# Performance work log

Hardware: AMD Instinct MI355X
Metric: run time of the kernel (lower is better)

## Reference

```python
import jax, jax.numpy as jnp
import numpy as np

# dims derived from init_kwargs
N_NODES = 100000            # type_mask.shape[0]
N0, N1 = 60000, 40000       # nodes per type
F0, F1 = 128, 64            # feats_dim_list
HID = 64                    # hidden_dim (= in_dim of layer1)
HEADS = 8
OUT = 16
ATTN_VEC = 128
E = 250000                  # metapath instances per metapath
L = 3                       # nodes per metapath instance (2 edge types)
NG = 8192                   # nodes in each minibatch DGL graph
B = 8192                    # number of target nodes
ETYPES = [[0, 1], [2, 3]]   # etypes_list; num_edge_type=4, RotatE0 -> 2 base relations


def setup_inputs() -> dict:
    ks = jax.random.split(jax.random.key(0), 20)
    g = lambda k, s, sc=1.0: sc * jax.random.normal(k, s, dtype=jnp.float32)
    return {
        "feat0": g(ks[0], (N0, F0)),
        "feat1": g(ks[1], (N1, F1)),
        "W0": g(ks[2], (HID, F0), 0.12),
        "b0": jnp.zeros((HID,), jnp.float32),
        "W1": g(ks[3], (HID, F1), 0.15),
        "b1": jnp.zeros((HID,), jnp.float32),
        "r_vec": g(ks[4], (2, HID // 2, 2), 0.2),
        "attn0": g(ks[5], (HEADS, HID), 0.2),
        "attn1": g(ks[6], (HEADS, HID), 0.2),
        "fc1_w": g(ks[7], (ATTN_VEC, HEADS * HID), 0.06),
        "fc1_b": jnp.zeros((ATTN_VEC,), jnp.float32),
        "fc2_w": g(ks[8], (1, ATTN_VEC), 0.1),
        "fc_w": g(ks[9], (OUT, HEADS * HID), 0.06),
        "fc_b": jnp.zeros((OUT,), jnp.float32),
        "idx0": jnp.arange(N0, dtype=jnp.int32),                 # type-0 node ids (contiguous block)
        "idx1": jnp.arange(N1, dtype=jnp.int32) + N0,            # type-1 node ids (offset block)
        "mp0_indices": jax.random.randint(ks[10], (E, L), 0, N_NODES, dtype=jnp.int32),
        "mp0_dst": jax.random.randint(ks[11], (E,), 0, NG, dtype=jnp.int32),
        "mp0_target": jax.random.randint(ks[12], (B,), 0, NG, dtype=jnp.int32),
        "mp1_indices": jax.random.randint(ks[13], (E, L), 0, N_NODES, dtype=jnp.int32),
        "mp1_dst": jax.random.randint(ks[14], (E,), 0, NG, dtype=jnp.int32),
        "mp1_target": jax.random.randint(ks[15], (B,), 0, NG, dtype=jnp.int32),
    }


def _cmul(a, b):
    # complex multiply on trailing dim of size 2
    re = a[..., 0] * b[..., 0] - a[..., 1] * b[..., 1]
    im = a[..., 0] * b[..., 1] + a[..., 1] * b[..., 0]
    return jnp.stack([re, im], axis=-1)


def reference(feat0, feat1, W0, b0, W1, b1, r_vec, attn0, attn1,
              fc1_w, fc1_b, fc2_w, fc_w, fc_b,
              idx0, idx1,
              mp0_indices, mp0_dst, mp0_target,
              mp1_indices, mp1_dst, mp1_target):
    # per-node-type linear scattered into a dense [N, HID] table (dropout=0 / eval)
    tf = jnp.zeros((N_NODES, HID), jnp.float32)
    tf = tf.at[idx0].set(feat0 @ W0.T + b0)
    tf = tf.at[idx1].set(feat1 @ W1.T + b1)

    # RotatE0: unit-modulus normalize, then double relations with conjugates
    rv = r_vec / jnp.linalg.norm(r_vec, axis=-1, keepdims=True)          # [2, HID//2, 2]
    conj = rv * jnp.array([1.0, -1.0], rv.dtype)
    rv_full = jnp.stack([rv, conj], axis=1).reshape(-1, HID // 2, 2)     # [4, HID//2, 2]

    def metapath(indices, dst, target, attn, etypes):
        edata = tf[indices].reshape(E, L, HID // 2, 2)   # gather metapath instances
        # suffix products of rotations: final[i] = prod_{j>=i} r[etypes[j]], final[L-1]=1
        final = [jnp.stack([jnp.ones(HID // 2, jnp.float32),
                            jnp.zeros(HID // 2, jnp.float32)], -1)]
        for i in range(L - 2, -1, -1):
            final.insert(0, _cmul(final[0], rv_full[etypes[i]]))
        finals = jnp.stack(final, axis=0)                # [L, HID//2, 2]
        edata = _cmul(edata, finals)                     # rotate every path position
        h = edata.reshape(E, L, HID).mean(axis=1)        # [E, HID] instance encoding
        # node-level attention (heads share h: torch tiles hidden across heads)
        a = jax.nn.leaky_relu(h @ attn.T, 0.01)          # [E, HEADS]
        m = jax.ops.segment_max(a, dst, num_segments=NG)
        ex = jnp.exp(a - m[dst])
        s = jax.ops.segment_sum(ex, dst, num_segments=NG)
        an = ex / s[dst]                                 # edge softmax per destination
        eft = jnp.einsum('eh,ed->ehd', an, h)            # [E, HEADS, HID]
        ft = jax.ops.segment_sum(eft, dst, num_segments=NG)
        ret = ft[target].reshape(B, HEADS * HID)
        return jax.nn.elu(ret)

    out0 = metapath(mp0_indices, mp0_dst, mp0_target, attn0, ETYPES[0])
    out1 = metapath(mp1_indices, mp1_dst, mp1_target, attn1, ETYPES[1])

    # metapath-level attention
    outs = jnp.stack([out0, out1], axis=0)               # [P, B, HEADS*HID]
    s1 = jnp.tanh(outs @ fc1_w.T + fc1_b)                # [P, B, ATTN_VEC]
    beta = jax.nn.softmax((s1.mean(axis=1) @ fc2_w.T)[:, 0], axis=0)  # [P]
    hagg = jnp.einsum('p,pbf->bf', beta, outs)           # [B, HEADS*HID]
    logits = hagg @ fc_w.T + fc_b                        # [B, OUT]
    return logits, hagg
```

## Files before the change

kernel.cpp:

```cpp
#include <hip/hip_runtime.h>
#include <hip/hip_fp16.h>
#include <math.h>

#define NNODES 100000
#define NT0 60000
#define NT1 40000
#define FD0 128
#define FD1 64
#define HID 64
#define HEADS 8
#define OUTD 16
#define AVEC 128
#define NE 250000
#define NG 8192
#define NB 8192

typedef _Float16 half8v __attribute__((ext_vector_type(8)));
typedef float f32x4 __attribute__((ext_vector_type(4)));

#define OFF_TF16    0ull
#define OFF_FINALS  3200000ull
#define OFF_A       3200512ull
#define OFF_ACC     3203584ull
#define OFF_BETA    3203840ull
#define OFF_FC1H    3204096ull
#define OFF_P       3236864ull
#define OFF_SORTED  5636864ull
#define OFF_COUNTS  7636864ull
#define OFF_CNTT    7653248ull
#define OFF_CURS    7669632ull
#define OFF_OFFS    7686016ull
#define OFF_FT16    7702656ull

__global__ __launch_bounds__(256) void k_prep(const float* __restrict__ r_vec,
                       const float* __restrict__ attn0, const float* __restrict__ attn1,
                       float* __restrict__ finals, float* __restrict__ A,
                       float* __restrict__ acc, float* __restrict__ beta){
  __shared__ float2 fl[192];
  int t = threadIdx.x;
  if (t < 32){
    int j = t;
    const float2* rv = (const float2*)r_vec;
    float2 r0 = rv[j];
    float2 r1 = rv[32 + j];
    float n0 = rsqrtf(r0.x*r0.x + r0.y*r0.y);
    float n1 = rsqrtf(r1.x*r1.x + r1.y*r1.y);
    r0.x *= n0; r0.y *= n0; r1.x *= n1; r1.y *= n1;
    float2 rf1 = make_float2(r0.x, -r0.y);
    float2 rf3 = make_float2(r1.x, -r1.y);
    float2 F00 = make_float2(rf1.x*r0.x - rf1.y*r0.y, rf1.x*r0.y + rf1.y*r0.x);
    float2 F10 = make_float2(rf3.x*r1.x - rf3.y*r1.y, rf3.x*r1.y + rf3.y*r1.x);
    float2 one = make_float2(1.f, 0.f);
    float2* F = (float2*)finals;
    F[0*32+j] = F00; F[1*32+j] = rf1; F[2*32+j] = one;
    F[3*32+j] = F10; F[4*32+j] = rf3; F[5*32+j] = one;
    fl[0*32+j] = F00; fl[1*32+j] = rf1; fl[2*32+j] = one;
    fl[3*32+j] = F10; fl[4*32+j] = rf3; fl[5*32+j] = one;
  }
  __syncthreads();
  for (int idx = t; idx < 1536; idx += 256){
    int pair = idx & 31, k = (idx >> 5) & 7, pi = idx >> 8;
    const float* at = (pi >= 3) ? attn1 : attn0;
    float2 f = fl[pi*32 + pair];
    float a0 = at[k*64 + 2*pair], a1 = at[k*64 + 2*pair + 1];
    A[(pi*8+k)*64 + 2*pair]     = (f.x*a0 + f.y*a1) * (1.f/3.f);
    A[(pi*8+k)*64 + 2*pair + 1] = (f.x*a1 - f.y*a0) * (1.f/3.f);
  }
  acc[t] = 0.f;
  if (t < 2) beta[t] = 0.f;
}

__global__ void k_cvtw(const float* __restrict__ fc1_w, __half* __restrict__ fc1h){
  int t = blockIdx.x*blockDim.x + threadIdx.x;
  fc1h[t] = __float2half(fc1_w[t]);
}

__global__ __launch_bounds__(256) void k_transform2(const float* __restrict__ feat0,
                  const float* __restrict__ W0v, const float* __restrict__ b0v,
                  const int* __restrict__ idx0,
                  const float* __restrict__ feat1, const float* __restrict__ W1v,
                  const float* __restrict__ b1v, const int* __restrict__ idx1,
                  __half* __restrict__ tf16){
  __shared__ float An[64][34];
  __shared__ float Bn[64][34];
  const int nb0 = (NT0 + 63)/64;
  int bid = blockIdx.x;
  const float *feat, *W, *bias; const int* idx; int n_nodes, F, m0;
  if (bid < nb0){ feat=feat0; W=W0v; bias=b0v; idx=idx0; n_nodes=NT0; F=FD0; m0=bid*64; }
  else { feat=feat1; W=W1v; bias=b1v; idx=idx1; n_nodes=NT1; F=FD1; m0=(bid-nb0)*64; }
  int t = threadIdx.x;
  int tx = t & 15;
  int ty = t >> 4;
  int Fq = F >> 2;

  float acc[4][4];
  #pragma unroll
  for (int i = 0; i < 4; ++i)
    #pragma unroll
    for (int j = 0; j < 4; ++j) acc[i][j] = 0.f;

  const float4* feat4 = (const float4*)feat;
  const float4* W4 = (const float4*)W;

  for (int k0 = 0; k0 < F; k0 += 32){
    #pragma unroll
    for (int qq = 0; qq < 2; ++qq){
      int q = t + qq*256;
      int m = q >> 3, kq = q & 7;
      int gm = m0 + m; if (gm > n_nodes - 1) gm = n_nodes - 1;
      float4 v = feat4[(size_t)gm*Fq + (k0 >> 2) + kq];
      *(float2*)&An[m][kq*4]     = make_float2(v.x, v.y);
      *(float2*)&An[m][kq*4 + 2] = make_float2(v.z, v.w);
    }
    #pragma unroll
    for (int qq = 0; qq < 2; ++qq){
      int q = t + qq*256;
      int d = q >> 3, kq = q & 7;
      float4 v = W4[(size_t)d*Fq + (k0 >> 2) + kq];
      *(float2*)&Bn[d][kq*4]     = make_float2(v.x, v.y);
      *(float2*)&Bn[d][kq*4 + 2] = make_float2(v.z, v.w);
    }
    __syncthreads();
    #pragma unroll 8
    for (int kk2 = 0; kk2 < 16; ++kk2){
      float2 a2[4], b2[4];
      #pragma unroll
      for (int i = 0; i < 4; ++i) a2[i] = *(const float2*)&An[tx + 16*i][kk2*2];
      #pragma unroll
      for (int j = 0; j < 4; ++j) b2[j] = *(const float2*)&Bn[ty*4 + j][kk2*2];
      #pragma unroll
      for (int i = 0; i < 4; ++i)
        #pragma unroll
        for (int j = 0; j < 4; ++j)
          acc[i][j] += a2[i].x*b2[j].x + a2[i].y*b2[j].y;
    }
    __syncthreads();
  }

  float4 bv = *(const float4*)&bias[ty*4];
  #pragma unroll
  for (int i = 0; i < 4; ++i){
    int gm = m0 + tx + 16*i;
    if (gm < n_nodes){
      union { __half2 h2[2]; uint2 u; } pk;
      pk.h2[0] = __floats2half2_rn(acc[i][0] + bv.x, acc[i][1] + bv.y);
      pk.h2[1] = __floats2half2_rn(acc[i][2] + bv.z, acc[i][3] + bv.w);
      *(uint2*)&tf16[(size_t)idx[gm]*HID + ty*4] = pk.u;
    }
  }
}

__global__ __launch_bounds__(256) void k_pmat(const __half* __restrict__ tf16,
                                              const float* __restrict__ A,
                                              __half* __restrict__ P){
  __shared__ float tfl[64][65];
  __shared__ float Al[48][65];
  int t = threadIdx.x;
  int n0 = blockIdx.x * 64;
  for (int q = t; q < 3072; q += 256) Al[q >> 6][q & 63] = A[q];
  const __half2* tfh = (const __half2*)(tf16 + (size_t)n0*64);
  for (int q = t; q < 2048; q += 256){
    int n = q >> 5, dq = q & 31;
    float2 v = make_float2(0.f, 0.f);
    if (n0 + n < NNODES) v = __half22float2(tfh[n*32 + dq]);
    tfl[n][dq*2] = v.x; tfl[n][dq*2+1] = v.y;
  }
  __syncthreads();
  int nl = t >> 2, q = t & 3;
  float s[12];
  #pragma unroll
  for (int c = 0; c < 12; ++c) s[c] = 0.f;
  #pragma unroll 4
  for (int d = 0; d < 64; ++d){
    float tv = tfl[nl][d];
    #pragma unroll
    for (int c = 0; c < 12; ++c) s[c] += tv * Al[q*12 + c][d];
  }
  int gn = n0 + nl;
  if (gn < NNODES){
    #pragma unroll
    for (int c = 0; c < 12; ++c){
      int cg = q*12 + c;
      int p = cg >= 24;
      int w = cg - p*24;
      P[(size_t)p*2400000 + (size_t)gn*24 + w] = __float2half(s[c]);
    }
  }
}

__global__ void k_zeroi(int* __restrict__ p, int n){
  int t = blockIdx.x*blockDim.x + threadIdx.x;
  if (t < n) p[t] = 0;
}

__global__ void k_hist3(const int* __restrict__ d0, const int* __restrict__ d1,
                        const int* __restrict__ t0, const int* __restrict__ t1,
                        int* __restrict__ counts, int* __restrict__ cntt){
  int e = blockIdx.x*blockDim.x + threadIdx.x;
  if (e < NE) atomicAdd(&counts[d0[e]], 1);
  else if (e < 2*NE) atomicAdd(&counts[NG + d1[e-NE]], 1);
  else if (e < 2*NE + NB) atomicAdd(&cntt[t0[e-2*NE]], 1);
  else if (e < 2*NE + 2*NB) atomicAdd(&cntt[NG + t1[e-2*NE-NB]], 1);
}

__global__ __launch_bounds__(1024) void k_scan(const int* __restrict__ counts,
                                               int* __restrict__ offs,
                                               int* __restrict__ curs){
  __shared__ int lds[1024];
  int t = threadIdx.x;
  int base = t*16;
  int v[16]; int sum = 0;
  #pragma unroll
  for (int i = 0; i < 16; ++i){ v[i] = counts[base+i]; sum += v[i]; }
  lds[t] = sum;
  __syncthreads();
  for (int off = 1; off < 1024; off <<= 1){
    int x = (t >= off) ? lds[t-off] : 0;
    __syncthreads();
    lds[t] += x;
    __syncthreads();
  }
  int excl = lds[t] - sum;
  #pragma unroll
  for (int i = 0; i < 16; ++i){ offs[base+i] = excl; excl += v[i]; curs[base+i] = 0; }
  if (t == 1023) offs[2*NG] = excl;
}

__global__ void k_scatter2(const int* __restrict__ m0, const int* __restrict__ d0,
                           const int* __restrict__ m1, const int* __restrict__ d1,
                           const int* __restrict__ offs, int* __restrict__ curs,
                           int4* __restrict__ sorted){
  int e = blockIdx.x*blockDim.x + threadIdx.x;
  if (e >= 2*NE) return;
  const int* mp; int d;
  if (e < NE){ mp = m0 + (size_t)e*3; d = d0[e]; }
  else { mp = m1 + (size_t)(e-NE)*3; d = NG + d1[e-NE]; }
  int pos = offs[d] + atomicAdd(&curs[d], 1);
  sorted[pos] = make_int4(mp[0], mp[1], mp[2], 0);
}

__global__ __launch_bounds__(64) void k_seg(const __half* __restrict__ tf16,
                                            const __half* __restrict__ P,
                                            const int4* __restrict__ sorted,
                                            const int* __restrict__ offs,
                                            const float* __restrict__ finals,
                                            __half* __restrict__ ft16o){
  int bid = blockIdx.x;
  int p = bid >> 13;
  int lane = threadIdx.x;
  int hw = lane >> 5, j = lane & 31;
  int start = offs[bid], end = offs[bid+1];
  __half2* ftw = (__half2*)(ft16o + (size_t)bid*512);
  if (start == end){
    #pragma unroll
    for (int kk = 0; kk < 4; ++kk) ftw[(hw*4+kk)*32 + j] = __floats2half2_rn(0.f, 0.f);
    return;
  }
  const float2* F2 = (const float2*)(finals + p*192);
  float2 f0 = F2[j], f1 = F2[32 + j];
  const __half2* tfh = (const __half2*)tf16;
  const __half* Pp = P + (size_t)p*2400000;

  __shared__ int4 ndb[64];
  __shared__ float wb[64][8];

  float s[8], ur[8], ui[8];
  #pragma unroll
  for (int k = 0; k < 8; ++k){ s[k] = 0.f; ur[k] = 0.f; ui[k] = 0.f; }

  for (int c = start; c < end; c += 64){
    int n = end - c; if (n > 64) n = 64;
    if (lane < n){
      int4 nd = sorted[c + lane];
      ndb[lane] = nd;
      float4 rA = *(const float4*)(Pp + (size_t)nd.x*24);
      float4 rB = *(const float4*)(Pp + (size_t)nd.y*24 + 8);
      float4 rC = *(const float4*)(Pp + (size_t)nd.z*24 + 16);
      const __half2* ha = (const __half2*)&rA;
      const __half2* hb = (const __half2*)&rB;
      const __half2* hc = (const __half2*)&rC;
      float w[8];
      #pragma unroll
      for (int m = 0; m < 4; ++m){
        float2 va = __half22float2(ha[m]);
        float2 vb = __half22float2(hb[m]);
        float2 vc = __half22float2(hc[m]);
        float x0 = va.x + vb.x + vc.x;
        float x1 = va.y + vb.y + vc.y;
        x0 = x0 > 0.f ? x0 : 0.01f*x0;
        x1 = x1 > 0.f ? x1 : 0.01f*x1;
        w[2*m]   = __expf(x0);
        w[2*m+1] = __expf(x1);
      }
      *(float4*)&wb[lane][0] = make_float4(w[0], w[1], w[2], w[3]);
      *(float4*)&wb[lane][4] = make_float4(w[4], w[5], w[6], w[7]);
    }
    __syncthreads();
    int cend = c + n;
    for (int i = c + hw; i < cend; i += 2){
      int e = i - c;
      int4 nd = ndb[e];
      float4 wlo = *(const float4*)&wb[e][0];
      float4 whi = *(const float4*)&wb[e][4];
      float2 v0 = __half22float2(tfh[(size_t)nd.x*32 + j]);
      float2 v1 = __half22float2(tfh[(size_t)nd.y*32 + j]);
      float2 v2 = __half22float2(tfh[(size_t)nd.z*32 + j]);
      float hre = (v0.x*f0.x - v0.y*f0.y) + (v1.x*f1.x - v1.y*f1.y) + v2.x;
      float him = (v0.x*f0.y + v0.y*f0.x) + (v1.x*f1.y + v1.y*f1.x) + v2.y;
      ur[0] += wlo.x*hre; ui[0] += wlo.x*him; s[0] += wlo.x;
      ur[1] += wlo.y*hre; ui[1] += wlo.y*him; s[1] += wlo.y;
      ur[2] += wlo.z*hre; ui[2] += wlo.z*him; s[2] += wlo.z;
      ur[3] += wlo.w*hre; ui[3] += wlo.w*him; s[3] += wlo.w;
      ur[4] += whi.x*hre; ui[4] += whi.x*him; s[4] += whi.x;
      ur[5] += whi.y*hre; ui[5] += whi.y*him; s[5] += whi.y;
      ur[6] += whi.z*hre; ui[6] += whi.z*him; s[6] += whi.z;
      ur[7] += whi.w*hre; ui[7] += whi.w*him; s[7] += whi.w;
    }
    __syncthreads();
  }
  #pragma unroll
  for (int k = 0; k < 8; ++k){
    ur[k] += __shfl_xor(ur[k], 32);
    ui[k] += __shfl_xor(ui[k], 32);
    s[k]  += __shfl_xor(s[k], 32);
  }
  #pragma unroll
  for (int kk = 0; kk < 4; ++kk){
    int k = hw*4 + kk;
    float inv = 1.f / (3.f * s[k]);
    float re = ur[k]*inv, im = ui[k]*inv;
    re = re > 0.f ? re : expm1f(re);
    im = im > 0.f ? im : expm1f(im);
    ftw[k*32 + j] = __floats2half2_rn(re, im);
  }
}

__global__ __launch_bounds__(256) void k_s1g(const __half* __restrict__ ft16o,
                                             const int* __restrict__ cntt,
                                             const __half* __restrict__ fc1h,
                                             const float* __restrict__ fc1_b,
                                             float* __restrict__ acc_p){
  int bid = blockIdx.x;
  int p  = bid >> 8;
  int rb = bid & 255;
  int t = threadIdx.x;
  int w = t >> 6, l = t & 63;
  int rowbase = rb*32 + (w & 1)*16;
  int colbase = (w >> 1)*64;
  int lr = l & 15, lk = l >> 4;

  const half8v* Ab = (const half8v*)(ft16o + ((size_t)p*NG + rowbase)*512);
  f32x4 acc[4] = {{0.f,0.f,0.f,0.f},{0.f,0.f,0.f,0.f},
                  {0.f,0.f,0.f,0.f},{0.f,0.f,0.f,0.f}};

  #pragma unroll 4
  for (int kk = 0; kk < 16; ++kk){
    half8v a = Ab[(size_t)lr*64 + kk*4 + lk];
    #pragma unroll
    for (int ct = 0; ct < 4; ++ct){
      const half8v* Bb = (const half8v*)(fc1h + (size_t)(colbase + ct*16 + lr)*512);
      half8v b = Bb[kk*4 + lk];
      acc[ct] = __builtin_amdgcn_mfma_f32_16x16x32_f16(a, b, acc[ct], 0, 0, 0);
    }
  }

  float cf[4];
  #pragma unroll
  for (int r = 0; r < 4; ++r)
    cf[r] = (float)cntt[p*NG + rowbase + lk*4 + r];
  #pragma unroll
  for (int ct = 0; ct < 4; ++ct){
    int col = colbase + ct*16 + lr;
    float bv = fc1_b[col];
    float sv = 0.f;
    #pragma unroll
    for (int r = 0; r < 4; ++r)
      sv += cf[r] * tanhf(acc[ct][r] + bv);
    sv += __shfl_xor(sv, 16);
    sv += __shfl_xor(sv, 32);
    if (l < 16) atomicAdd(&acc_p[p*128 + col], sv);
  }
}

__global__ void k_beta(const float* __restrict__ acc, const float* __restrict__ fc2_w,
                       float* __restrict__ beta){
  int t = threadIdx.x;
  float s0 = acc[t]*fc2_w[t] + acc[t+64]*fc2_w[t+64];
  float s1 = acc[128+t]*fc2_w[t] + acc[192+t]*fc2_w[t+64];
  #pragma unroll
  for (int mask = 1; mask < 64; mask <<= 1){
    s0 += __shfl_xor(s0, mask, 64);
    s1 += __shfl_xor(s1, mask, 64);
  }
  if (t == 0){
    float z0 = s0 / (float)NB, z1 = s1 / (float)NB;
    float mz = fmaxf(z0, z1);
    float e0 = expf(z0 - mz), e1 = expf(z1 - mz);
    float inv = 1.f / (e0 + e1);
    beta[0] = e0*inv; beta[1] = e1*inv;
  }
}

__global__ void k_final(const __half* __restrict__ ft0, const __half* __restrict__ ft1,
                        const int* __restrict__ tgt0, const int* __restrict__ tgt1,
                        const float* __restrict__ beta, const float* __restrict__ fc_w,
                        const float* __restrict__ fc_b, float* __restrict__ d_out){
  __shared__ float lds[512];
  int b = blockIdx.x, t = threadIdx.x;
  float b0 = beta[0], b1 = beta[1];
  int g0 = tgt0[b], g1 = tgt1[b];
  float v0 = __half2float(ft0[(size_t)g0*512 + t]);
  float v1 = __half2float(ft1[(size_t)g1*512 + t]);
  float h = b0*v0 + b1*v1;
  lds[t] = h;
  d_out[(size_t)NB*OUTD + (size_t)b*512 + t] = h;
  __syncthreads();
  int o = t >> 5, j = t & 31;
  float s = 0.f;
  const float* w = fc_w + o*512;
  for (int d = j; d < 512; d += 32) s += lds[d]*w[d];
  #pragma unroll
  for (int mask = 1; mask < 32; mask <<= 1) s += __shfl_xor(s, mask, 32);
  if (j == 0) d_out[(size_t)b*OUTD + o] = s + fc_b[o];
}

extern "C" void kernel_launch(void* const* d_in, const int* in_sizes, int n_in,
                              void* d_out, int out_size, void* d_ws, size_t ws_size,
                              hipStream_t stream){
  const float* feat0  = (const float*)d_in[0];
  const float* feat1  = (const float*)d_in[1];
  const float* W0     = (const float*)d_in[2];
  const float* b0     = (const float*)d_in[3];
  const float* W1     = (const float*)d_in[4];
  const float* b1     = (const float*)d_in[5];
  const float* r_vec  = (const float*)d_in[6];
  const float* attn0  = (const float*)d_in[7];
  const float* attn1  = (const float*)d_in[8];
  const float* fc1_w  = (const float*)d_in[9];
  const float* fc1_b  = (const float*)d_in[10];
  const float* fc2_w  = (const float*)d_in[11];
  const float* fc_w   = (const float*)d_in[12];
  const float* fc_b   = (const float*)d_in[13];
  const int*   idx0   = (const int*)d_in[14];
  const int*   idx1   = (const int*)d_in[15];
  const int*   mpi0   = (const int*)d_in[16];
  const int*   mdst0  = (const int*)d_in[17];
  const int*   mtgt0  = (const int*)d_in[18];
  const int*   mpi1   = (const int*)d_in[19];
  const int*   mdst1  = (const int*)d_in[20];
  const int*   mtgt1  = (const int*)d_in[21];

  float* ws      = (float*)d_ws;
  __half* tf16   = (__half*)(ws + OFF_TF16);
  float* finals  = ws + OFF_FINALS;
  float* Amat    = ws + OFF_A;
  float* acc     = ws + OFF_ACC;
  float* beta    = ws + OFF_BETA;
  __half* fc1h   = (__half*)(ws + OFF_FC1H);
  __half* P      = (__half*)(ws + OFF_P);
  int4*  sorted  = (int4*)(ws + OFF_SORTED);
  int*   counts  = (int*)(ws + OFF_COUNTS);
  int*   cntt    = (int*)(ws + OFF_CNTT);
  int*   curs    = (int*)(ws + OFF_CURS);
  int*   offs    = (int*)(ws + OFF_OFFS);
  __half* ft16o  = (__half*)(ws + OFF_FT16);
  __half* ft0h   = ft16o;
  __half* ft1h   = ft16o + (size_t)NG*512;

  k_prep<<<1, 256, 0, stream>>>(r_vec, attn0, attn1, finals, Amat, acc, beta);
  k_cvtw<<<256, 256, 0, stream>>>(fc1_w, fc1h);
  k_zeroi<<<128, 256, 0, stream>>>(counts, 4*NG);
  k_hist3<<<(2*NE + 2*NB + 255)/256, 256, 0, stream>>>(mdst0, mdst1, mtgt0, mtgt1,
                                                       counts, cntt);
  k_scan<<<1, 1024, 0, stream>>>(counts, offs, curs);
  k_scatter2<<<(2*NE + 255)/256, 256, 0, stream>>>(mpi0, mdst0, mpi1, mdst1,
                                                   offs, curs, sorted);

  k_transform2<<<(NT0 + 63)/64 + (NT1 + 63)/64, 256, 0, stream>>>(
      feat0, W0, b0, idx0, feat1, W1, b1, idx1, tf16);
  k_pmat<<<(NNODES + 63)/64, 256, 0, stream>>>(tf16, Amat, P);

  k_seg<<<2*NG, 64, 0, stream>>>(tf16, P, sorted, offs, finals, ft16o);

  k_s1g<<<512, 256, 0, stream>>>(ft16o, cntt, fc1h, fc1_b, acc);
  k_beta<<<1, 64, 0, stream>>>(acc, fc2_w, beta);
  k_final<<<NB, 512, 0, stream>>>(ft0h, ft1h, mtgt0, mtgt1, beta, fc_w, fc_b,
                                  (float*)d_out);
}
```

Baseline: 254.9 us.

## Fold attention projection into transform weights and compute with MFMA

```diff
diff --git a/kernel.cpp b/kernel.cpp
--- a/kernel.cpp
+++ b/kernel.cpp
@@ -20,23 +20,30 @@
 
 #define OFF_TF16    0ull
 #define OFF_FINALS  3200000ull
-#define OFF_A       3200512ull
-#define OFF_ACC     3203584ull
-#define OFF_BETA    3203840ull
-#define OFF_FC1H    3204096ull
-#define OFF_P       3236864ull
-#define OFF_SORTED  5636864ull
-#define OFF_COUNTS  7636864ull
-#define OFF_CNTT    7653248ull
-#define OFF_CURS    7669632ull
-#define OFF_OFFS    7686016ull
-#define OFF_FT16    7702656ull
-
-__global__ __launch_bounds__(256) void k_prep(const float* __restrict__ r_vec,
-                       const float* __restrict__ attn0, const float* __restrict__ attn1,
-                       float* __restrict__ finals, float* __restrict__ A,
-                       float* __restrict__ acc, float* __restrict__ beta){
+#define OFF_ACC     3200512ull
+#define OFF_BETA    3200768ull
+#define OFF_WC0     3201024ull
+#define OFF_WC1     3208192ull
+#define OFF_BC0     3211776ull
+#define OFF_BC1     3211904ull
+#define OFF_FC1H    3212032ull
+#define OFF_P       3244800ull
+#define OFF_SORTED  5644800ull
+#define OFF_COUNTS  7644800ull
+#define OFF_CNTT    7661184ull
+#define OFF_CURS    7677568ull
+#define OFF_OFFS    7693952ull
+#define OFF_FT16    7710592ull
+
+__global__ __launch_bounds__(256) void k_wprep(const float* __restrict__ r_vec,
+     const float* __restrict__ attn0, const float* __restrict__ attn1,
+     const float* __restrict__ W0v, const float* __restrict__ b0v,
+     const float* __restrict__ W1v, const float* __restrict__ b1v,
+     float* __restrict__ finals, __half* __restrict__ wc0, float* __restrict__ bc0,
+     __half* __restrict__ wc1, float* __restrict__ bc1,
+     float* __restrict__ acc, float* __restrict__ beta){
   __shared__ float2 fl[192];
+  __shared__ float Ash[48][66];
   int t = threadIdx.x;
   if (t < 32){
     int j = t;
@@ -63,8 +70,46 @@
     const float* at = (pi >= 3) ? attn1 : attn0;
     float2 f = fl[pi*32 + pair];
     float a0 = at[k*64 + 2*pair], a1 = at[k*64 + 2*pair + 1];
-    A[(pi*8+k)*64 + 2*pair]     = (f.x*a0 + f.y*a1) * (1.f/3.f);
-    A[(pi*8+k)*64 + 2*pair + 1] = (f.x*a1 - f.y*a0) * (1.f/3.f);
+    Ash[pi*8+k][2*pair]     = (f.x*a0 + f.y*a1) * (1.f/3.f);
+    Ash[pi*8+k][2*pair + 1] = (f.x*a1 - f.y*a0) * (1.f/3.f);
+  }
+  __syncthreads();
+  for (int q = t; q < 112*128; q += 256){
+    int c = q >> 7, f = q & 127;
+    float v;
+    if (c < 64) v = W0v[c*128 + f];
+    else {
+      float s = 0.f;
+      #pragma unroll 8
+      for (int d = 0; d < 64; ++d) s += Ash[c-64][d] * W0v[d*128 + f];
+      v = s;
+    }
+    wc0[q] = __float2half(v);
+  }
+  for (int q = t; q < 112*64; q += 256){
+    int c = q >> 6, f = q & 63;
+    float v;
+    if (c < 64) v = W1v[c*64 + f];
+    else {
+      float s = 0.f;
+      #pragma unroll 8
+      for (int d = 0; d < 64; ++d) s += Ash[c-64][d] * W1v[d*64 + f];
+      v = s;
+    }
+    wc1[q] = __float2half(v);
+  }
+  if (t < 112){
+    float s0, s1;
+    if (t < 64){ s0 = b0v[t]; s1 = b1v[t]; }
+    else {
+      s0 = 0.f; s1 = 0.f;
+      #pragma unroll 8
+      for (int d = 0; d < 64; ++d){
+        s0 += Ash[t-64][d] * b0v[d];
+        s1 += Ash[t-64][d] * b1v[d];
+      }
+    }
+    bc0[t] = s0; bc1[t] = s1;
   }
   acc[t] = 0.f;
   if (t < 2) beta[t] = 0.f;
@@ -75,115 +120,66 @@
   fc1h[t] = __float2half(fc1_w[t]);
 }
 
-__global__ __launch_bounds__(256) void k_transform2(const float* __restrict__ feat0,
-                  const float* __restrict__ W0v, const float* __restrict__ b0v,
-                  const int* __restrict__ idx0,
-                  const float* __restrict__ feat1, const float* __restrict__ W1v,
-                  const float* __restrict__ b1v, const int* __restrict__ idx1,
-                  __half* __restrict__ tf16){
-  __shared__ float An[64][34];
-  __shared__ float Bn[64][34];
+__global__ __launch_bounds__(256) void k_tform(const float* __restrict__ feat0,
+      const int* __restrict__ idx0, const float* __restrict__ feat1,
+      const int* __restrict__ idx1,
+      const __half* __restrict__ wc0, const float* __restrict__ bc0,
+      const __half* __restrict__ wc1, const float* __restrict__ bc1,
+      __half* __restrict__ tf16, __half* __restrict__ P){
   const int nb0 = (NT0 + 63)/64;
   int bid = blockIdx.x;
-  const float *feat, *W, *bias; const int* idx; int n_nodes, F, m0;
-  if (bid < nb0){ feat=feat0; W=W0v; bias=b0v; idx=idx0; n_nodes=NT0; F=FD0; m0=bid*64; }
-  else { feat=feat1; W=W1v; bias=b1v; idx=idx1; n_nodes=NT1; F=FD1; m0=(bid-nb0)*64; }
+  const float* feat; const int* idx; const __half* wc; const float* bc;
+  int n_nodes, F, m0;
+  if (bid < nb0){ feat=feat0; idx=idx0; wc=wc0; bc=bc0; n_nodes=NT0; F=FD0; m0=bid*64; }
+  else { feat=feat1; idx=idx1; wc=wc1; bc=bc1; n_nodes=NT1; F=FD1; m0=(bid-nb0)*64; }
+  __shared__ int idxs[64];
   int t = threadIdx.x;
-  int tx = t & 15;
-  int ty = t >> 4;
-  int Fq = F >> 2;
-
-  float acc[4][4];
-  #pragma unroll
-  for (int i = 0; i < 4; ++i)
-    #pragma unroll
-    for (int j = 0; j < 4; ++j) acc[i][j] = 0.f;
-
-  const float4* feat4 = (const float4*)feat;
-  const float4* W4 = (const float4*)W;
-
-  for (int k0 = 0; k0 < F; k0 += 32){
-    #pragma unroll
-    for (int qq = 0; qq < 2; ++qq){
-      int q = t + qq*256;
-      int m = q >> 3, kq = q & 7;
-      int gm = m0 + m; if (gm > n_nodes - 1) gm = n_nodes - 1;
-      float4 v = feat4[(size_t)gm*Fq + (k0 >> 2) + kq];
-      *(float2*)&An[m][kq*4]     = make_float2(v.x, v.y);
-      *(float2*)&An[m][kq*4 + 2] = make_float2(v.z, v.w);
-    }
-    #pragma unroll
-    for (int qq = 0; qq < 2; ++qq){
-      int q = t + qq*256;
-      int d = q >> 3, kq = q & 7;
-      float4 v = W4[(size_t)d*Fq + (k0 >> 2) + kq];
-      *(float2*)&Bn[d][kq*4]     = make_float2(v.x, v.y);
-      *(float2*)&Bn[d][kq*4 + 2] = make_float2(v.z, v.w);
-    }
-    __syncthreads();
-    #pragma unroll 8
-    for (int kk2 = 0; kk2 < 16; ++kk2){
-      float2 a2[4], b2[4];
-      #pragma unroll
-      for (int i = 0; i < 4; ++i) a2[i] = *(const float2*)&An[tx + 16*i][kk2*2];
-      #pragma unroll
-      for (int j = 0; j < 4; ++j) b2[j] = *(const float2*)&Bn[ty*4 + j][kk2*2];
-      #pragma unroll
-      for (int i = 0; i < 4; ++i)
-        #pragma unroll
-        for (int j = 0; j < 4; ++j)
-          acc[i][j] += a2[i].x*b2[j].x + a2[i].y*b2[j].y;
-    }
-    __syncthreads();
-  }
-
-  float4 bv = *(const float4*)&bias[ty*4];
-  #pragma unroll
-  for (int i = 0; i < 4; ++i){
-    int gm = m0 + tx + 16*i;
-    if (gm < n_nodes){
-      union { __half2 h2[2]; uint2 u; } pk;
-      pk.h2[0] = __floats2half2_rn(acc[i][0] + bv.x, acc[i][1] + bv.y);
-      pk.h2[1] = __floats2half2_rn(acc[i][2] + bv.z, acc[i][3] + bv.w);
-      *(uint2*)&tf16[(size_t)idx[gm]*HID + ty*4] = pk.u;
-    }
-  }
-}
-
-__global__ __launch_bounds__(256) void k_pmat(const __half* __restrict__ tf16,
-                                              const float* __restrict__ A,
-                                              __half* __restrict__ P){
-  __shared__ float tfl[64][65];
-  __shared__ float Al[48][65];
-  int t = threadIdx.x;
-  int n0 = blockIdx.x * 64;
-  for (int q = t; q < 3072; q += 256) Al[q >> 6][q & 63] = A[q];
-  const __half2* tfh = (const __half2*)(tf16 + (size_t)n0*64);
-  for (int q = t; q < 2048; q += 256){
-    int n = q >> 5, dq = q & 31;
-    float2 v = make_float2(0.f, 0.f);
-    if (n0 + n < NNODES) v = __half22float2(tfh[n*32 + dq]);
-    tfl[n][dq*2] = v.x; tfl[n][dq*2+1] = v.y;
+  if (t < 64){
+    int gm = m0 + t; if (gm > n_nodes - 1) gm = n_nodes - 1;
+    idxs[t] = idx[gm];
   }
   __syncthreads();
-  int nl = t >> 2, q = t & 3;
-  float s[12];
-  #pragma unroll
-  for (int c = 0; c < 12; ++c) s[c] = 0.f;
-  #pragma unroll 4
-  for (int d = 0; d < 64; ++d){
-    float tv = tfl[nl][d];
-    #pragma unroll
-    for (int c = 0; c < 12; ++c) s[c] += tv * Al[q*12 + c][d];
-  }
-  int gn = n0 + nl;
-  if (gn < NNODES){
-    #pragma unroll
-    for (int c = 0; c < 12; ++c){
-      int cg = q*12 + c;
-      int p = cg >= 24;
-      int w = cg - p*24;
-      P[(size_t)p*2400000 + (size_t)gn*24 + w] = __float2half(s[c]);
+  int w = t >> 6, l = t & 63;
+  int lr = l & 15, lk = l >> 4;
+  int gr = m0 + w*16 + lr; if (gr > n_nodes - 1) gr = n_nodes - 1;
+  const float* arow = feat + (size_t)gr*F;
+
+  f32x4 acc7[7];
+  #pragma unroll
+  for (int ct = 0; ct < 7; ++ct) acc7[ct] = (f32x4){0.f,0.f,0.f,0.f};
+
+  int nk = F >> 5;
+  for (int kk = 0; kk < nk; ++kk){
+    int koff = kk*32 + lk*8;
+    float4 ua = *(const float4*)(arow + koff);
+    float4 ub = *(const float4*)(arow + koff + 4);
+    half8v a = {(_Float16)ua.x,(_Float16)ua.y,(_Float16)ua.z,(_Float16)ua.w,
+                (_Float16)ub.x,(_Float16)ub.y,(_Float16)ub.z,(_Float16)ub.w};
+    #pragma unroll
+    for (int ct = 0; ct < 7; ++ct){
+      half8v b = *(const half8v*)(wc + (size_t)(ct*16 + lr)*F + koff);
+      acc7[ct] = __builtin_amdgcn_mfma_f32_16x16x32_f16(a, b, acc7[ct], 0, 0, 0);
+    }
+  }
+
+  #pragma unroll
+  for (int ct = 0; ct < 7; ++ct){
+    int col = ct*16 + lr;
+    float bv = bc[col];
+    #pragma unroll
+    for (int r = 0; r < 4; ++r){
+      int nl = w*16 + lk*4 + r;
+      int gm = m0 + nl;
+      if (gm < n_nodes){
+        __half hv = __float2half(acc7[ct][r] + bv);
+        int gn = idxs[nl];
+        if (col < 64) tf16[(size_t)gn*64 + col] = hv;
+        else {
+          int cg = col - 64;
+          int p = cg >= 24;
+          P[(size_t)p*2400000 + (size_t)gn*24 + (cg - p*24)] = hv;
+        }
+      }
     }
   }
 }
@@ -264,9 +260,9 @@
   __shared__ int4 ndb[64];
   __shared__ float wb[64][8];
 
-  float s[8], ur[8], ui[8];
-  #pragma unroll
-  for (int k = 0; k < 8; ++k){ s[k] = 0.f; ur[k] = 0.f; ui[k] = 0.f; }
+  float sA[8], ur[8], ui[8];
+  #pragma unroll
+  for (int k = 0; k < 8; ++k){ sA[k] = 0.f; ur[k] = 0.f; ui[k] = 0.f; }
 
   for (int c = start; c < end; c += 64){
     int n = end - c; if (n > 64) n = 64;
@@ -292,6 +288,8 @@
         w[2*m]   = __expf(x0);
         w[2*m+1] = __expf(x1);
       }
+      #pragma unroll
+      for (int k = 0; k < 8; ++k) sA[k] += w[k];
       *(float4*)&wb[lane][0] = make_float4(w[0], w[1], w[2], w[3]);
       *(float4*)&wb[lane][4] = make_float4(w[4], w[5], w[6], w[7]);
     }
@@ -307,14 +305,14 @@
       float2 v2 = __half22float2(tfh[(size_t)nd.z*32 + j]);
       float hre = (v0.x*f0.x - v0.y*f0.y) + (v1.x*f1.x - v1.y*f1.y) + v2.x;
       float him = (v0.x*f0.y + v0.y*f0.x) + (v1.x*f1.y + v1.y*f1.x) + v2.y;
-      ur[0] += wlo.x*hre; ui[0] += wlo.x*him; s[0] += wlo.x;
-      ur[1] += wlo.y*hre; ui[1] += wlo.y*him; s[1] += wlo.y;
-      ur[2] += wlo.z*hre; ui[2] += wlo.z*him; s[2] += wlo.z;
-      ur[3] += wlo.w*hre; ui[3] += wlo.w*him; s[3] += wlo.w;
-      ur[4] += whi.x*hre; ui[4] += whi.x*him; s[4] += whi.x;
-      ur[5] += whi.y*hre; ui[5] += whi.y*him; s[5] += whi.y;
-      ur[6] += whi.z*hre; ui[6] += whi.z*him; s[6] += whi.z;
-      ur[7] += whi.w*hre; ui[7] += whi.w*him; s[7] += whi.w;
+      ur[0] += wlo.x*hre; ui[0] += wlo.x*him;
+      ur[1] += wlo.y*hre; ui[1] += wlo.y*him;
+      ur[2] += wlo.z*hre; ui[2] += wlo.z*him;
+      ur[3] += wlo.w*hre; ui[3] += wlo.w*him;
+      ur[4] += whi.x*hre; ui[4] += whi.x*him;
+      ur[5] += whi.y*hre; ui[5] += whi.y*him;
+      ur[6] += whi.z*hre; ui[6] += whi.z*him;
+      ur[7] += whi.w*hre; ui[7] += whi.w*him;
     }
     __syncthreads();
   }
@@ -322,12 +320,15 @@
   for (int k = 0; k < 8; ++k){
     ur[k] += __shfl_xor(ur[k], 32);
     ui[k] += __shfl_xor(ui[k], 32);
-    s[k]  += __shfl_xor(s[k], 32);
+    float v = sA[k];
+    #pragma unroll
+    for (int mask = 1; mask < 64; mask <<= 1) v += __shfl_xor(v, mask);
+    sA[k] = v;
   }
   #pragma unroll
   for (int kk = 0; kk < 4; ++kk){
     int k = hw*4 + kk;
-    float inv = 1.f / (3.f * s[k]);
+    float inv = 1.f / (3.f * sA[k]);
     float re = ur[k]*inv, im = ui[k]*inv;
     re = re > 0.f ? re : expm1f(re);
     im = im > 0.f ? im : expm1f(im);
@@ -453,9 +454,12 @@
   float* ws      = (float*)d_ws;
   __half* tf16   = (__half*)(ws + OFF_TF16);
   float* finals  = ws + OFF_FINALS;
-  float* Amat    = ws + OFF_A;
   float* acc     = ws + OFF_ACC;
   float* beta    = ws + OFF_BETA;
+  __half* wc0    = (__half*)(ws + OFF_WC0);
+  __half* wc1    = (__half*)(ws + OFF_WC1);
+  float* bc0     = ws + OFF_BC0;
+  float* bc1     = ws + OFF_BC1;
   __half* fc1h   = (__half*)(ws + OFF_FC1H);
   __half* P      = (__half*)(ws + OFF_P);
   int4*  sorted  = (int4*)(ws + OFF_SORTED);
@@ -467,7 +471,8 @@
   __half* ft0h   = ft16o;
   __half* ft1h   = ft16o + (size_t)NG*512;
 
-  k_prep<<<1, 256, 0, stream>>>(r_vec, attn0, attn1, finals, Amat, acc, beta);
+  k_wprep<<<1, 256, 0, stream>>>(r_vec, attn0, attn1, W0, b0, W1, b1,
+                                 finals, wc0, bc0, wc1, bc1, acc, beta);
   k_cvtw<<<256, 256, 0, stream>>>(fc1_w, fc1h);
   k_zeroi<<<128, 256, 0, stream>>>(counts, 4*NG);
   k_hist3<<<(2*NE + 2*NB + 255)/256, 256, 0, stream>>>(mdst0, mdst1, mtgt0, mtgt1,
@@ -476,9 +481,8 @@
   k_scatter2<<<(2*NE + 255)/256, 256, 0, stream>>>(mpi0, mdst0, mpi1, mdst1,
                                                    offs, curs, sorted);
 
-  k_transform2<<<(NT0 + 63)/64 + (NT1 + 63)/64, 256, 0, stream>>>(
-      feat0, W0, b0, idx0, feat1, W1, b1, idx1, tf16);
-  k_pmat<<<(NNODES + 63)/64, 256, 0, stream>>>(tf16, Amat, P);
+  k_tform<<<(NT0 + 63)/64 + (NT1 + 63)/64, 256, 0, stream>>>(
+      feat0, idx0, feat1, idx1, wc0, bc0, wc1, bc1, tf16, P);
 
   k_seg<<<2*NG, 64, 0, stream>>>(tf16, P, sorted, offs, finals, ft16o);
 
```

New measurement: 275.5 us. 8.0% more time.
